# Performance work log

Measured on AMD Instinct MI355X. Metric: run time of the kernel, lower is better.

## Reference

```python
import jax, jax.numpy as jnp
import numpy as np

N_HEAD = 16
ROPE_BASE = 10000.0


def rope_cache(T, dim):
    half = dim // 2
    inv_freq = 1.0 / (ROPE_BASE ** (jnp.arange(half, dtype=jnp.float32) / half))
    freqs = jnp.arange(T, dtype=jnp.float32)[:, None] * inv_freq[None, :]  # [T, half]
    cos = jnp.repeat(jnp.cos(freqs), 2, axis=-1)  # [T, dim]
    sin = jnp.repeat(jnp.sin(freqs), 2, axis=-1)
    return cos, sin


def apply_rope(x, cos, sin):
    # x: [B, H, T, hd]; cos/sin: [T, hd] broadcast over B,H
    x1 = x[..., ::2]
    x2 = x[..., 1::2]
    x_rot = jnp.stack([-x2, x1], axis=-1).reshape(x.shape)
    return x * cos + x_rot * sin


def setup_inputs() -> dict:
    key = jax.random.key(0)
    k1, k2, k3, k4 = jax.random.split(key, 4)
    C = 1024
    x = jax.random.normal(k1, (2, 2048, C), jnp.float32)
    w_qkv = jax.random.normal(k2, (3 * C, C), jnp.float32) * 0.02
    w_out = jax.random.normal(k3, (C, C), jnp.float32) * 0.02
    b_out = jax.random.normal(k4, (C,), jnp.float32) * 0.02
    return {"x": x, "w_qkv": w_qkv, "w_out": w_out, "b_out": b_out}


def reference(x, w_qkv, w_out, b_out):
    B, T, C = x.shape
    H = N_HEAD
    hd = C // H
    qkv = x @ w_qkv.T                              # [B, T, 3C]
    qkv = qkv.reshape(B, T, 3, H, hd).transpose(2, 0, 3, 1, 4)  # [3, B, H, T, hd]
    q, k, v = qkv[0], qkv[1], qkv[2]
    cos, sin = rope_cache(T, hd)
    q = apply_rope(q, cos, sin)
    k = apply_rope(k, cos, sin)
    scale = hd ** (-0.5)
    scores = jnp.einsum('bhqd,bhkd->bhqk', q, k) * scale       # [B, H, T, T]
    causal = jnp.tril(jnp.ones((T, T), dtype=bool))
    scores = jnp.where(causal, scores, jnp.float32(-jnp.inf))
    att = jax.nn.softmax(scores, axis=-1)
    out = jnp.einsum('bhqk,bhkd->bhqd', att, v)                # [B, H, T, hd]
    out = out.transpose(0, 2, 1, 3).reshape(B, T, C)
    return out @ w_out.T + b_out
```

## Files before the change

### kernel.cpp

```cpp
#include <hip/hip_runtime.h>
#include <math.h>

namespace {

typedef __attribute__((ext_vector_type(8))) short s16x8;
typedef __attribute__((ext_vector_type(4))) float f32x4;
typedef unsigned int u32;
typedef unsigned short u16;

constexpr int B_ = 2;
constexpr int T_ = 2048;
constexpr int C_ = 1024;
constexpr int H_ = 16;
constexpr float L2E = 1.44269504088896340736f;

__device__ inline u16 f2bf(float x) {
    __bf16 h = (__bf16)x;
    return __builtin_bit_cast(u16, h);
}
__device__ inline u32 packbf2(float a, float b) {
    return (u32)f2bf(a) | ((u32)f2bf(b) << 16);
}
__device__ inline void gload_lds16(const void* g, void* lds) {
    __builtin_amdgcn_global_load_lds(
        (const __attribute__((address_space(1))) unsigned int*)g,
        (__attribute__((address_space(3))) unsigned int*)lds, 16, 0, 0);
}

__global__ __launch_bounds__(256) void tab_k(float2* __restrict__ cs) {
    int idx = blockIdx.x * 256 + threadIdx.x;
    int t = idx >> 5, i = idx & 31;
    float inv = 1.0f / powf(10000.0f, (float)i / 32.0f);
    float ang = (float)t * inv;
    cs[idx] = make_float2(cosf(ang), sinf(ang));
}

__global__ __launch_bounds__(256)
void cvt_k(const float4* __restrict__ x, const float4* __restrict__ wq,
           const float4* __restrict__ wo, uint2* __restrict__ xb,
           uint2* __restrict__ wqb, uint2* __restrict__ wob) {
    int i = blockIdx.x * 256 + threadIdx.x;
    const float4* s;
    uint2* d;
    int j;
    if (i < 1048576) { s = x; d = xb; j = i; }
    else if (i < 1048576 + 786432) { s = wq; d = wqb; j = i - 1048576; }
    else { s = wo; d = wob; j = i - (1048576 + 786432); }
    float4 v = s[j];
    d[j] = make_uint2(packbf2(v.x, v.y), packbf2(v.z, v.w));
}

__global__ __launch_bounds__(256)
void qkv_mfma_k(const u16* __restrict__ xb, const u16* __restrict__ wqb,
                const float2* __restrict__ cs, u16* __restrict__ qb,
                u16* __restrict__ kb, u16* __restrict__ vt) {
    __shared__ char lds[16384];
    const int tid = threadIdx.x;
    const int w = tid >> 6, lane = tid & 63;
    const int c = lane & 15, g = lane >> 4;
    const int n0 = blockIdx.x * 128, m0 = blockIdx.y * 128;
    const int wr = w >> 1, wc = w & 1;

    f32x4 acc[4][4];
#pragma unroll
    for (int i = 0; i < 4; ++i)
#pragma unroll
        for (int j = 0; j < 4; ++j) acc[i][j] = (f32x4){0.f, 0.f, 0.f, 0.f};

    const u16* Ab = xb + (size_t)m0 * C_;
    const u16* Bb = wqb + (size_t)n0 * C_;
    const int srow = tid >> 2, sslot = tid & 3;

    for (int k0 = 0; k0 < C_; k0 += 32) {
        __syncthreads();
#pragma unroll
        for (int call = 0; call < 2; ++call) {
            int r = call * 64 + srow;
            int ds = sslot ^ (r & 3);
            gload_lds16(Ab + (size_t)r * C_ + k0 + ds * 8, lds + call * 4096 + w * 1024);
            gload_lds16(Bb + (size_t)r * C_ + k0 + ds * 8, lds + 8192 + call * 4096 + w * 1024);
        }
        __syncthreads();
        s16x8 aF[4], bF[4];
#pragma unroll
        for (int mf = 0; mf < 4; ++mf) {
            int row = wr * 64 + mf * 16 + c;
            aF[mf] = *(const s16x8*)(lds + row * 64 + ((g ^ (row & 3)) * 16));
        }
#pragma unroll
        for (int nf = 0; nf < 4; ++nf) {
            int row = wc * 64 + nf * 16 + c;
            bF[nf] = *(const s16x8*)(lds + 8192 + row * 64 + ((g ^ (row & 3)) * 16));
        }
#pragma unroll
        for (int mf = 0; mf < 4; ++mf)
#pragma unroll
            for (int nf = 0; nf < 4; ++nf)
                acc[mf][nf] = __builtin_amdgcn_mfma_f32_16x16x32_bf16(aF[mf], bF[nf], acc[mf][nf], 0, 0, 0);
    }

    const int sec = n0 >> 10;
    const int h = ((n0 & 1023) >> 6) + wc;
    const int b = m0 >> 11;
    const int t0w = (m0 & 2047) + wr * 64;
    const int bh = b * H_ + h;
    if (sec < 2) {
        u16* dst = (sec == 0) ? qb : kb;
        const float qs = (sec == 0) ? 0.125f : 1.0f;
#pragma unroll
        for (int nf = 0; nf < 4; ++nf) {
            int d = nf * 16 + c;
            int ibase = nf * 8 + (c >> 1);
#pragma unroll
            for (int mf = 0; mf < 4; ++mf) {
#pragma unroll
                for (int r = 0; r < 4; ++r) {
                    int t = t0w + mf * 16 + g * 4 + r;
                    float own = acc[mf][nf][r];
                    float partner = __shfl_xor(own, 1);
                    float2 csv = cs[t * 32 + ibase];
                    float rot = (d & 1) ? (own * csv.x + partner * csv.y)
                                        : (own * csv.x - partner * csv.y);
                    rot *= qs;
                    float rothi = __shfl_xor(rot, 1);
                    if (!(d & 1))
                        *(u32*)(dst + ((size_t)bh * T_ + t) * 64 + d) = packbf2(rot, rothi);
                }
            }
        }
    } else {
#pragma unroll
        for (int nf = 0; nf < 4; ++nf) {
            int d = nf * 16 + c;
#pragma unroll
            for (int mf = 0; mf < 4; ++mf) {
                int tb = t0w + mf * 16 + g * 4;
                u32 lo = packbf2(acc[mf][nf][0], acc[mf][nf][1]);
                u32 hi = packbf2(acc[mf][nf][2], acc[mf][nf][3]);
                *(uint2*)(vt + ((size_t)bh * 64 + d) * T_ + tb) = make_uint2(lo, hi);
            }
        }
    }
}

__global__ __launch_bounds__(256)
void flash_mfma_k(const u16* __restrict__ qb, const u16* __restrict__ kb,
                  const u16* __restrict__ vt, u16* __restrict__ attb) {
    __shared__ char lds[32768];
    char* Qs = lds;
    char* Ks = lds + 8192;
    char* Vs = lds + 16384;
    char* Ps = lds + 24576;
    const int tid = threadIdx.x, w = tid >> 6, lane = tid & 63;
    const int c = lane & 15, g = lane >> 4;
    const int bh = blockIdx.x;
    const int qi = 31 - blockIdx.y;
    const int q0 = qi * 64, q0w = q0 + w * 16;
    const u16* Qg = qb + ((size_t)bh * T_ + q0) * 64;
    const u16* Kg = kb + (size_t)bh * T_ * 64;
    const u16* Vg = vt + (size_t)bh * 64 * T_;

#pragma unroll
    for (int call = 0; call < 2; ++call) {
        int row = call * 32 + (tid >> 3);
        int ds = (tid & 7) ^ (row & 7);
        gload_lds16(Qg + (size_t)row * 64 + ds * 8, Qs + call * 4096 + w * 1024);
    }
    __syncthreads();

    s16x8 bQ[2];
#pragma unroll
    for (int kc = 0; kc < 2; ++kc) {
        int row = w * 16 + c;
        bQ[kc] = *(const s16x8*)(Qs + row * 128 + (((kc * 4 + g) ^ (row & 7)) * 16));
    }

    float m_ = -INFINITY, l_ = 0.f;
    f32x4 accO[4];
#pragma unroll
    for (int j = 0; j < 4; ++j) accO[j] = (f32x4){0.f, 0.f, 0.f, 0.f};

    const int nt = qi + 1;
    for (int kt = 0; kt < nt; ++kt) {
        __syncthreads();
        {
            int row = tid >> 3, slot = tid & 7;
#pragma unroll
            for (int call = 0; call < 2; ++call) {
                int r = call * 32 + row;
                int ds = slot ^ (r & 7);
                gload_lds16(Kg + (size_t)(kt * 64 + r) * 64 + ds * 8, Ks + call * 4096 + w * 1024);
                gload_lds16(Vg + (size_t)r * T_ + kt * 64 + ds * 8, Vs + call * 4096 + w * 1024);
            }
        }
        __syncthreads();

        f32x4 S[4];
#pragma unroll
        for (int mf = 0; mf < 4; ++mf) S[mf] = (f32x4){0.f, 0.f, 0.f, 0.f};
        s16x8 aK[4][2];
#pragma unroll
        for (int mf = 0; mf < 4; ++mf)
#pragma unroll
            for (int kc = 0; kc < 2; ++kc) {
                int row = mf * 16 + c;
                aK[mf][kc] = *(const s16x8*)(Ks + row * 128 + (((kc * 4 + g) ^ (row & 7)) * 16));
            }
#pragma unroll
        for (int kc = 0; kc < 2; ++kc)
#pragma unroll
            for (int mf = 0; mf < 4; ++mf)
                S[mf] = __builtin_amdgcn_mfma_f32_16x16x32_bf16(aK[mf][kc], bQ[kc], S[mf], 0, 0, 0);

        if (kt == qi) {
#pragma unroll
            for (int mf = 0; mf < 4; ++mf)
#pragma unroll
                for (int r = 0; r < 4; ++r) {
                    int kvg = kt * 64 + mf * 16 + g * 4 + r;
                    if (kvg > q0w + c) S[mf][r] = -INFINITY;
                }
        }

        float mx = -INFINITY;
#pragma unroll
        for (int mf = 0; mf < 4; ++mf)
#pragma unroll
            for (int r = 0; r < 4; ++r) mx = fmaxf(mx, S[mf][r]);
        mx = fmaxf(mx, __shfl_xor(mx, 16));
        mx = fmaxf(mx, __shfl_xor(mx, 32));
        float alpha = 1.0f;
        if (!__all(mx - m_ <= 8.0f)) {
            float mnew = fmaxf(m_, mx);
            alpha = exp2f((m_ - mnew) * L2E);
            m_ = mnew;
#pragma unroll
            for (int r = 0; r < 4; ++r) {
                float ar = __shfl(alpha, g * 4 + r);
#pragma unroll
                for (int nd = 0; nd < 4; ++nd) accO[nd][r] *= ar;
            }
        }
        float sum = 0.f;
#pragma unroll
        for (int mf = 0; mf < 4; ++mf)
#pragma unroll
            for (int r = 0; r < 4; ++r) {
                float p = exp2f((S[mf][r] - m_) * L2E);
                S[mf][r] = p;
                sum += p;
            }
        sum += __shfl_xor(sum, 16);
        sum += __shfl_xor(sum, 32);
        l_ = l_ * alpha + sum;

#pragma unroll
        for (int mf = 0; mf < 4; ++mf)
#pragma unroll
            for (int p2 = 0; p2 < 2; ++p2) {
                u32 v = packbf2(S[mf][2 * p2], S[mf][2 * p2 + 1]);
                int off = (mf * 16 + g * 4 + p2 * 2) * 2;
                *(u32*)(Ps + w * 2048 + c * 128 + (off ^ ((c & 7) << 4))) = v;
            }
        __threadfence_block();

        s16x8 aP[2], bV[4][2];
#pragma unroll
        for (int kc = 0; kc < 2; ++kc)
            aP[kc] = *(const s16x8*)(Ps + w * 2048 + c * 128 + (((kc * 4 + g) ^ (c & 7)) * 16));
#pragma unroll
        for (int nd = 0; nd < 4; ++nd)
#pragma unroll
            for (int kc = 0; kc < 2; ++kc) {
                int row = nd * 16 + c;
                bV[nd][kc] = *(const s16x8*)(Vs + row * 128 + (((kc * 4 + g) ^ (row & 7)) * 16));
            }
#pragma unroll
        for (int kc = 0; kc < 2; ++kc)
#pragma unroll
            for (int nd = 0; nd < 4; ++nd)
                accO[nd] = __builtin_amdgcn_mfma_f32_16x16x32_bf16(aP[kc], bV[nd][kc], accO[nd], 0, 0, 0);
    }

    const int hh = bh & 15;
    const int bb = bh >> 4;
#pragma unroll
    for (int r = 0; r < 4; ++r) {
        float linv = 1.0f / __shfl(l_, g * 4 + r);
        int t = q0w + g * 4 + r;
        size_t rowb = ((size_t)bb * T_ + t) * C_ + hh * 64;
#pragma unroll
        for (int nd = 0; nd < 4; ++nd)
            attb[rowb + nd * 16 + c] = f2bf(accO[nd][r] * linv);
    }
}

__global__ __launch_bounds__(256)
void proj_mfma_k(const u16* __restrict__ attb, const u16* __restrict__ wob,
                 const float* __restrict__ bias, float* __restrict__ out) {
    __shared__ char lds[16384];
    const int tid = threadIdx.x;
    const int w = tid >> 6, lane = tid & 63;
    const int c = lane & 15, g = lane >> 4;
    const int n0 = blockIdx.x * 128, m0 = blockIdx.y * 128;
    const int wr = w >> 1, wc = w & 1;

    f32x4 acc[4][4];
#pragma unroll
    for (int i = 0; i < 4; ++i)
#pragma unroll
        for (int j = 0; j < 4; ++j) acc[i][j] = (f32x4){0.f, 0.f, 0.f, 0.f};

    const u16* Ab = attb + (size_t)m0 * C_;
    const u16* Bb = wob + (size_t)n0 * C_;
    const int srow = tid >> 2, sslot = tid & 3;

    for (int k0 = 0; k0 < C_; k0 += 32) {
        __syncthreads();
#pragma unroll
        for (int call = 0; call < 2; ++call) {
            int r = call * 64 + srow;
            int ds = sslot ^ (r & 3);
            gload_lds16(Ab + (size_t)r * C_ + k0 + ds * 8, lds + call * 4096 + w * 1024);
            gload_lds16(Bb + (size_t)r * C_ + k0 + ds * 8, lds + 8192 + call * 4096 + w * 1024);
        }
        __syncthreads();
        s16x8 aF[4], bF[4];
#pragma unroll
        for (int mf = 0; mf < 4; ++mf) {
            int row = wr * 64 + mf * 16 + c;
            aF[mf] = *(const s16x8*)(lds + row * 64 + ((g ^ (row & 3)) * 16));
        }
#pragma unroll
        for (int nf = 0; nf < 4; ++nf) {
            int row = wc * 64 + nf * 16 + c;
            bF[nf] = *(const s16x8*)(lds + 8192 + row * 64 + ((g ^ (row & 3)) * 16));
        }
#pragma unroll
        for (int mf = 0; mf < 4; ++mf)
#pragma unroll
            for (int nf = 0; nf < 4; ++nf)
                acc[mf][nf] = __builtin_amdgcn_mfma_f32_16x16x32_bf16(aF[mf], bF[nf], acc[mf][nf], 0, 0, 0);
    }

#pragma unroll
    for (int nf = 0; nf < 4; ++nf) {
        int n = n0 + wc * 64 + nf * 16 + c;
        float bv = bias[n];
#pragma unroll
        for (int mf = 0; mf < 4; ++mf)
#pragma unroll
            for (int r = 0; r < 4; ++r) {
                int mrow = m0 + wr * 64 + mf * 16 + g * 4 + r;
                out[(size_t)mrow * C_ + n] = acc[mf][nf][r] + bv;
            }
    }
}

}

extern "C" void kernel_launch(void* const* d_in, const int* in_sizes, int n_in,
                              void* d_out, int out_size, void* d_ws, size_t ws_size,
                              hipStream_t stream) {
    const float* x     = (const float*)d_in[0];
    const float* w_qkv = (const float*)d_in[1];
    const float* w_out = (const float*)d_in[2];
    const float* b_out = (const float*)d_in[3];
    float* out = (float*)d_out;

    char* ws = (char*)d_ws;
    float2* cs = (float2*)ws;
    u16* xb   = (u16*)(ws + 524288);
    u16* wqb  = (u16*)(ws + 524288 + 8388608);
    u16* wob  = (u16*)(ws + 524288 + 8388608 + 6291456);
    u16* qb   = (u16*)(ws + 17301504);
    u16* kb   = (u16*)(ws + 25690112);
    u16* vt   = (u16*)(ws + 34078720);
    u16* attb = (u16*)(ws + 42467328);

    tab_k<<<256, 256, 0, stream>>>(cs);
    cvt_k<<<8192, 256, 0, stream>>>((const float4*)x, (const float4*)w_qkv,
                                    (const float4*)w_out, (uint2*)xb, (uint2*)wqb, (uint2*)wob);
    qkv_mfma_k<<<dim3(24, 32), 256, 0, stream>>>(xb, wqb, cs, qb, kb, vt);
    flash_mfma_k<<<dim3(32, 32), 256, 0, stream>>>(qb, kb, vt, attb);
    proj_mfma_k<<<dim3(8, 32), 256, 0, stream>>>(attb, wob, b_out, out);
}
```

Measured before the change: 227.6 us.

## Double-buffer LDS tiles in QKV and output projection GEMMs, adjust swizzle

```diff
diff --git a/kernel.cpp b/kernel.cpp
--- a/kernel.cpp
+++ b/kernel.cpp
@@ -54,7 +54,7 @@
 void qkv_mfma_k(const u16* __restrict__ xb, const u16* __restrict__ wqb,
                 const float2* __restrict__ cs, u16* __restrict__ qb,
                 u16* __restrict__ kb, u16* __restrict__ vt) {
-    __shared__ char lds[16384];
+    __shared__ char lds[32768];
     const int tid = threadIdx.x;
     const int w = tid >> 6, lane = tid & 63;
     const int c = lane & 15, g = lane >> 4;
@@ -71,33 +71,44 @@
     const u16* Bb = wqb + (size_t)n0 * C_;
     const int srow = tid >> 2, sslot = tid & 3;
 
-    for (int k0 = 0; k0 < C_; k0 += 32) {
-        __syncthreads();
+    auto stage = [&](int k0, char* base) {
 #pragma unroll
         for (int call = 0; call < 2; ++call) {
             int r = call * 64 + srow;
-            int ds = sslot ^ (r & 3);
-            gload_lds16(Ab + (size_t)r * C_ + k0 + ds * 8, lds + call * 4096 + w * 1024);
-            gload_lds16(Bb + (size_t)r * C_ + k0 + ds * 8, lds + 8192 + call * 4096 + w * 1024);
-        }
-        __syncthreads();
+            int ds = sslot ^ ((r >> 1) & 3);
+            gload_lds16(Ab + (size_t)r * C_ + k0 + ds * 8, base + call * 4096 + w * 1024);
+            gload_lds16(Bb + (size_t)r * C_ + k0 + ds * 8, base + 8192 + call * 4096 + w * 1024);
+        }
+    };
+    auto compute = [&](const char* base) {
         s16x8 aF[4], bF[4];
 #pragma unroll
         for (int mf = 0; mf < 4; ++mf) {
             int row = wr * 64 + mf * 16 + c;
-            aF[mf] = *(const s16x8*)(lds + row * 64 + ((g ^ (row & 3)) * 16));
+            aF[mf] = *(const s16x8*)(base + row * 64 + ((g ^ ((row >> 1) & 3)) * 16));
         }
 #pragma unroll
         for (int nf = 0; nf < 4; ++nf) {
             int row = wc * 64 + nf * 16 + c;
-            bF[nf] = *(const s16x8*)(lds + 8192 + row * 64 + ((g ^ (row & 3)) * 16));
+            bF[nf] = *(const s16x8*)(base + 8192 + row * 64 + ((g ^ ((row >> 1) & 3)) * 16));
         }
 #pragma unroll
         for (int mf = 0; mf < 4; ++mf)
 #pragma unroll
             for (int nf = 0; nf < 4; ++nf)
                 acc[mf][nf] = __builtin_amdgcn_mfma_f32_16x16x32_bf16(aF[mf], bF[nf], acc[mf][nf], 0, 0, 0);
-    }
+    };
+
+    stage(0, lds);
+    __syncthreads();
+    int cur = 0;
+    for (int t = 0; t < 31; ++t) {
+        stage((t + 1) * 32, lds + ((cur ^ 1) << 14));
+        compute(lds + (cur << 14));
+        __syncthreads();
+        cur ^= 1;
+    }
+    compute(lds + (cur << 14));
 
     const int sec = n0 >> 10;
     const int h = ((n0 & 1023) >> 6) + wc;
@@ -298,7 +309,7 @@
 __global__ __launch_bounds__(256)
 void proj_mfma_k(const u16* __restrict__ attb, const u16* __restrict__ wob,
                  const float* __restrict__ bias, float* __restrict__ out) {
-    __shared__ char lds[16384];
+    __shared__ char lds[32768];
     const int tid = threadIdx.x;
     const int w = tid >> 6, lane = tid & 63;
     const int c = lane & 15, g = lane >> 4;
@@ -315,33 +326,44 @@
     const u16* Bb = wob + (size_t)n0 * C_;
     const int srow = tid >> 2, sslot = tid & 3;
 
-    for (int k0 = 0; k0 < C_; k0 += 32) {
-        __syncthreads();
+    auto stage = [&](int k0, char* base) {
 #pragma unroll
         for (int call = 0; call < 2; ++call) {
             int r = call * 64 + srow;
-            int ds = sslot ^ (r & 3);
-            gload_lds16(Ab + (size_t)r * C_ + k0 + ds * 8, lds + call * 4096 + w * 1024);
-            gload_lds16(Bb + (size_t)r * C_ + k0 + ds * 8, lds + 8192 + call * 4096 + w * 1024);
-        }
-        __syncthreads();
+            int ds = sslot ^ ((r >> 1) & 3);
+            gload_lds16(Ab + (size_t)r * C_ + k0 + ds * 8, base + call * 4096 + w * 1024);
+            gload_lds16(Bb + (size_t)r * C_ + k0 + ds * 8, base + 8192 + call * 4096 + w * 1024);
+        }
+    };
+    auto compute = [&](const char* base) {
         s16x8 aF[4], bF[4];
 #pragma unroll
         for (int mf = 0; mf < 4; ++mf) {
             int row = wr * 64 + mf * 16 + c;
-            aF[mf] = *(const s16x8*)(lds + row * 64 + ((g ^ (row & 3)) * 16));
+            aF[mf] = *(const s16x8*)(base + row * 64 + ((g ^ ((row >> 1) & 3)) * 16));
         }
 #pragma unroll
         for (int nf = 0; nf < 4; ++nf) {
             int row = wc * 64 + nf * 16 + c;
-            bF[nf] = *(const s16x8*)(lds + 8192 + row * 64 + ((g ^ (row & 3)) * 16));
+            bF[nf] = *(const s16x8*)(base + 8192 + row * 64 + ((g ^ ((row >> 1) & 3)) * 16));
         }
 #pragma unroll
         for (int mf = 0; mf < 4; ++mf)
 #pragma unroll
             for (int nf = 0; nf < 4; ++nf)
                 acc[mf][nf] = __builtin_amdgcn_mfma_f32_16x16x32_bf16(aF[mf], bF[nf], acc[mf][nf], 0, 0, 0);
-    }
+    };
+
+    stage(0, lds);
+    __syncthreads();
+    int cur = 0;
+    for (int t = 0; t < 31; ++t) {
+        stage((t + 1) * 32, lds + ((cur ^ 1) << 14));
+        compute(lds + (cur << 14));
+        __syncthreads();
+        cur ^= 1;
+    }
+    compute(lds + (cur << 14));
 
 #pragma unroll
     for (int nf = 0; nf < 4; ++nf) {
```

After: 224.0 us. No clear change (-1.6%).
